# Kernel tuning notes

Measured on AMD Instinct MI355X. Metric: run time of the kernel, lower is better.

## Reference

```python
import jax, jax.numpy as jnp
import numpy as np

T, N, E, V, D, H, Dh = 64, 2048, 8192, 64000, 128, 12, 10  # head_size = 128 // 12 = 10


def setup_inputs() -> dict:
    key = jax.random.key(0)
    ks = jax.random.split(key, 16)
    s = 1.0 / np.sqrt(D)
    return {
        "node_ids": jax.random.randint(ks[0], (T, N), 0, V, dtype=jnp.int32),
        "src": jax.random.randint(ks[1], (T, E), 0, N, dtype=jnp.int32),
        "dst": jax.random.randint(ks[2], (T, E), 0, N, dtype=jnp.int32),
        "edge_weights": jax.random.uniform(ks[3], (T, E), dtype=jnp.float32),
        "emb": jax.random.normal(ks[4], (V, D), dtype=jnp.float32) * 0.02,
        "Wp": jax.random.normal(ks[5], (D, D), dtype=jnp.float32) * s,
        "bp": jnp.zeros((D,), jnp.float32),
        "Wq": jax.random.normal(ks[6], (D, H * Dh), dtype=jnp.float32) * s,
        "bq": jnp.zeros((H * Dh,), jnp.float32),
        "Wk": jax.random.normal(ks[7], (D, H * Dh), dtype=jnp.float32) * s,
        "bk": jnp.zeros((H * Dh,), jnp.float32),
        "Wv": jax.random.normal(ks[8], (D, H * Dh), dtype=jnp.float32) * s,
        "bv": jnp.zeros((H * Dh,), jnp.float32),
        "Wo": jax.random.normal(ks[9], (H * Dh, 2), dtype=jnp.float32) * (1.0 / np.sqrt(H * Dh)),
        "bo": jnp.zeros((2,), jnp.float32),
    }


def reference(node_ids, src, dst, edge_weights, emb, Wp, bp, Wq, bq, Wk, bk, Wv, bv, Wo, bo):
    def propagate(x, s, d, w):
        # edge-weighted gather-multiply-scatter-add, then linear projection
        msg = x[s] * w[:, None]                                   # [E, D]
        n_hat = x + jax.ops.segment_sum(msg, d, num_segments=N)   # [N, D]
        return n_hat @ Wp + bp

    def step(carry, inp):
        ids, s, d, w = inp
        x = emb[ids]                       # [N, D] embedding lookup
        x = propagate(x, s, d, w)
        x = propagate(x, s, d, w)
        x = propagate(x, s, d, w)          # three rounds, as in SpatialEncoding.forward
        return carry, x

    _, node_emb = jax.lax.scan(step, None, (node_ids, src, dst, edge_weights))  # [T, N, D]

    # per-node temporal sequence: [N, T, D]
    seq = jnp.transpose(node_emb, (1, 0, 2))

    q = (seq @ Wq + bq).reshape(N, T, H, Dh)
    k = (seq @ Wk + bk).reshape(N, T, H, Dh)
    v = (seq @ Wv + bv).reshape(N, T, H, Dh)

    scale = 1.0 / jnp.sqrt(jnp.float32(Dh))
    scores = jnp.einsum('nthd,nshd->nhts', q, k) * scale          # [N, H, T, T]
    attn = jax.nn.softmax(scores, axis=-1)
    out = jnp.einsum('nhts,nshd->nthd', attn, v).reshape(N, T, H * Dh)  # [N, T, 120]

    # agg = cat over nodes -> [N*T, 120]; transpose(1,0).mean(-1) == mean over N*T axis
    agg = out.reshape(N * T, H * Dh).mean(axis=0)                 # [120]
    return agg @ Wo + bo                                          # [2]
```

## Files before the change

kernel.cpp:

```cpp
#include <hip/hip_runtime.h>
#include <stdint.h>

#define TT 64
#define NN 2048
#define EE 8192
#define DD 128
#define CAP 32

typedef __attribute__((ext_vector_type(8))) short bvec8;
typedef __attribute__((ext_vector_type(4))) float fvec4;

__device__ __forceinline__ float bf2f(uint16_t u){
  union { uint32_t i; float f; } v; v.i = ((uint32_t)u) << 16; return v.f;
}
__device__ __forceinline__ float lo16(uint32_t u){
  union { uint32_t i; float f; } v; v.i = u << 16; return v.f;
}
__device__ __forceinline__ float hi16(uint32_t u){
  union { uint32_t i; float f; } v; v.i = u & 0xffff0000u; return v.f;
}
__device__ __forceinline__ uint16_t f2bf(float f){
  union { float f; uint32_t i; } v; v.f = f;
  uint32_t r = v.i + 0x7fffu + ((v.i >> 16) & 1u);
  return (uint16_t)(r >> 16);
}
__device__ __forceinline__ uint32_t cvtpk(float lo, float hi){
  uint32_t r;
  asm("v_cvt_pk_bf16_f32 %0, %1, %2" : "=v"(r) : "v"(lo), "v"(hi));
  return r;
}
__device__ __forceinline__ fvec4 mfma16(bvec8 a, bvec8 b, fvec4 c){
  return __builtin_amdgcn_mfma_f32_16x16x32_bf16(a, b, c, 0, 0, 0);
}
__device__ __forceinline__ bvec8 pack8z(float a, float b, float c, float d){
  union { uint32_t u[4]; bvec8 v; } r;
  r.u[0] = cvtpk(a, b);
  r.u[1] = cvtpk(c, d);
  r.u[2] = 0u;
  r.u[3] = 0u;
  return r.v;
}

__global__ void k_init(const int* __restrict__ dst, int* __restrict__ cnt,
                       int* __restrict__ esw,
                       const float* __restrict__ Wp, const float* __restrict__ Wq,
                       const float* __restrict__ Wk, const float* __restrict__ Wv,
                       const float* __restrict__ bq, const float* __restrict__ bk,
                       const float* __restrict__ bv,
                       uint16_t* __restrict__ WpHi, uint16_t* __restrict__ WpLo,
                       uint16_t* __restrict__ QHi, float* __restrict__ biasPad,
                       const int* __restrict__ ids, const float* __restrict__ emb,
                       uint16_t* __restrict__ x){
  int bid = blockIdx.x;
  if (bid < 2048){
    int tid = bid * 256 + threadIdx.x;
    int t = tid >> 13, e = tid & (EE - 1);
    int d = dst[tid];
    int row = t * NN + d;
    int pos = atomicAdd(&cnt[row], 1);
    if (pos < CAP) esw[(size_t)row * 2 * CAP + 2 * pos] = e;
  } else if (bid < 2048 + 47){
    int tid = (bid - 2048) * 256 + threadIdx.x;
    if (tid < 2048){
      int lane = tid & 63, kc = (tid >> 6) & 3, ct = tid >> 8;
      int g = lane >> 4, l15 = lane & 15;
      #pragma unroll
      for (int j = 0; j < 8; ++j){
        int k = kc * 32 + g * 8 + j;
        int col = ct * 16 + l15;
        float v = Wp[k * DD + col];
        uint16_t h = f2bf(v);
        WpHi[(size_t)tid * 8 + j] = h;
        WpLo[(size_t)tid * 8 + j] = f2bf(v - bf2f(h));
      }
    } else if (tid < 2048 + 9216){
      int idx = tid - 2048;
      int lane = idx & 63, kc = (idx >> 6) & 3, t2 = idx >> 8;
      int h = t2 % 12, m = t2 / 12;
      const float* W = (m == 0) ? Wq : (m == 1) ? Wk : Wv;
      int g = lane >> 4, l15 = lane & 15;
      #pragma unroll
      for (int j = 0; j < 8; ++j){
        int k = kc * 32 + g * 8 + j;
        float v = (l15 < 10) ? W[k * 120 + h * 10 + l15] : 0.f;
        QHi[(size_t)idx * 8 + j] = f2bf(v);
      }
    } else if (tid < 2048 + 9216 + 576){
      int idx = tid - (2048 + 9216);
      int m = idx / 192, rest = idx % 192;
      int h = rest / 16, d = rest % 16;
      const float* B = (m == 0) ? bq : (m == 1) ? bk : bv;
      biasPad[idx] = (d < 10) ? B[h * 10 + d] : 0.f;
    }
  } else {
    int tid = (bid - 2095) * 256 + threadIdx.x;
    int row = tid >> 4, c8 = tid & 15;
    int id = ids[row];
    const float* er = emb + (size_t)id * DD + c8 * 8;
    float4 a = *(const float4*)er;
    float4 b = *(const float4*)(er + 4);
    union { uint32_t u[4]; bvec8 v; } o;
    o.u[0] = cvtpk(a.x, a.y);
    o.u[1] = cvtpk(a.z, a.w);
    o.u[2] = cvtpk(b.x, b.y);
    o.u[3] = cvtpk(b.z, b.w);
    *(bvec8*)(x + (size_t)row * DD + c8 * 8) = o.v;
  }
}

__global__ void k_sortconv(int* __restrict__ cnt, int* __restrict__ esw,
                           const int* __restrict__ srcA, const float* __restrict__ ewA){
  int row = blockIdx.x * 256 + threadIdx.x;
  if (row >= TT * NN) return;
  int t = row >> 11;
  int c = cnt[row]; if (c > CAP) c = CAP;
  cnt[row] = c;
  int* p = esw + (size_t)row * 2 * CAP;
  for (int i = 0; i < c; ++i){
    int mi = i, mv = p[2 * i];
    for (int j = i + 1; j < c; ++j){ int vj = p[2 * j]; if (vj < mv){ mv = vj; mi = j; } }
    if (mi != i){ p[2 * mi] = p[2 * i]; p[2 * i] = mv; }
  }
  const int* srcT = srcA + (size_t)t * EE;
  const float* ewT = ewA + (size_t)t * EE;
  for (int i = 0; i < c; ++i){
    int e = p[2 * i];
    p[2 * i]     = srcT[e];
    p[2 * i + 1] = __float_as_int(ewT[e]);
  }
}

__global__ __launch_bounds__(256, 4) void k_prop(const uint16_t* __restrict__ xin,
    uint16_t* __restrict__ xout, const int* __restrict__ cnt, const int* __restrict__ esw,
    const uint16_t* __restrict__ WHi, const uint16_t* __restrict__ WLo,
    const float* __restrict__ bp, int topt){
  __shared__ uint16_t lds[64 * 136];
  __shared__ int4 eplds[256];
  int vb = blockIdx.x;
  int b = ((vb & 7) << 8) | (vb >> 3);
  int t = b >> 5, n0 = (b & 31) << 6;
  int tid = threadIdx.x, w = tid >> 6, lane = tid & 63, g = lane >> 4, l15 = lane & 15;
  const uint16_t* xt = xin + (size_t)t * NN * DD;
  int baseRow = t * NN + n0;
  eplds[tid] = ((const int4*)(esw + (size_t)(baseRow + (tid >> 2)) * 2 * CAP))[tid & 3];
  int myc = (lane < 16) ? cnt[baseRow + w * 16 + lane] : 0;
  __syncthreads();
  #pragma unroll 2
  for (int i = 0; i < 16; ++i){
    int r = w * 16 + i;
    int n = n0 + r;
    uint32_t u = *(const uint32_t*)(xt + (size_t)n * DD + (lane << 1));
    int c = __shfl(myc, i);
    const int4* epr = &eplds[r * 4];
    int4 q0 = epr[0], q1 = epr[1], q2 = epr[2], q3 = epr[3];
    int sj[8]   = {q0.x, q0.z, q1.x, q1.z, q2.x, q2.z, q3.x, q3.z};
    float wj[8] = {__int_as_float(q0.y), __int_as_float(q0.w),
                   __int_as_float(q1.y), __int_as_float(q1.w),
                   __int_as_float(q2.y), __int_as_float(q2.w),
                   __int_as_float(q3.y), __int_as_float(q3.w)};
    uint32_t xs[8];
    float wf[8];
    #pragma unroll
    for (int j = 0; j < 8; ++j){
      int s = (j < c) ? sj[j] : 0;
      wf[j] = (j < c) ? wj[j] : 0.f;
      xs[j] = *(const uint32_t*)(xt + (size_t)s * DD + (lane << 1));
    }
    float a0 = lo16(u);
    float a1 = hi16(u);
    #pragma unroll
    for (int j = 0; j < 8; ++j){
      a0 = fmaf(wf[j], lo16(xs[j]), a0);
      a1 = fmaf(wf[j], hi16(xs[j]), a1);
    }
    if (c > 8){
      int rowg = baseRow + r;
      for (int j = 8; j < c; ++j){
        int s = esw[(size_t)rowg * 2 * CAP + 2 * j];
        float wt = __int_as_float(esw[(size_t)rowg * 2 * CAP + 2 * j + 1]);
        uint32_t us = *(const uint32_t*)(xt + (size_t)s * DD + (lane << 1));
        a0 = fmaf(wt, lo16(us), a0);
        a1 = fmaf(wt, hi16(us), a1);
      }
    }
    *(uint32_t*)&lds[r * 136 + (lane << 1)] = cvtpk(a0, a1);
  }
  __syncthreads();
  bvec8 afr[4];
  int arow = w * 16 + l15;
  #pragma unroll
  for (int kc = 0; kc < 4; ++kc)
    afr[kc] = *(const bvec8*)&lds[arow * 136 + kc * 32 + g * 8];
  fvec4 acc[8];
  #pragma unroll
  for (int i = 0; i < 8; ++i) acc[i] = fvec4{0.f, 0.f, 0.f, 0.f};
  #pragma unroll
  for (int kc = 0; kc < 4; ++kc){
    #pragma unroll
    for (int ct = 0; ct < 8; ++ct){
      size_t base = ((size_t)(ct * 4 + kc) * 64 + lane) * 8;
      acc[ct] = mfma16(afr[kc], *(const bvec8*)&WHi[base], acc[ct]);
      acc[ct] = mfma16(afr[kc], *(const bvec8*)&WLo[base], acc[ct]);
    }
  }
  __syncthreads();
  #pragma unroll
  for (int ct = 0; ct < 8; ++ct){
    int col = ct * 16 + l15;
    float bias = bp[col];
    uint32_t c01 = cvtpk(acc[ct][0] + bias, acc[ct][1] + bias);
    uint32_t c23 = cvtpk(acc[ct][2] + bias, acc[ct][3] + bias);
    int r = w * 16 + g * 4;
    lds[(r + 0) * 136 + col] = (uint16_t)c01;
    lds[(r + 1) * 136 + col] = (uint16_t)(c01 >> 16);
    lds[(r + 2) * 136 + col] = (uint16_t)c23;
    lds[(r + 3) * 136 + col] = (uint16_t)(c23 >> 16);
  }
  __syncthreads();
  #pragma unroll
  for (int p = 0; p < 4; ++p){
    int chunk = p * 256 + tid, r = chunk >> 4, c8 = chunk & 15;
    bvec8 v = *(const bvec8*)&lds[r * 136 + c8 * 8];
    size_t dstoff;
    if (topt == 0) dstoff = ((size_t)t * NN + n0 + r) * DD + c8 * 8;
    else           dstoff = (((size_t)(n0 + r)) * TT + t) * DD + c8 * 8;
    *(bvec8*)(xout + dstoff) = v;
  }
}

__global__ __launch_bounds__(256, 3) void k_attn(const uint16_t* __restrict__ x3,
    const uint16_t* __restrict__ QHi, const float* __restrict__ biasPad,
    float* __restrict__ partials){
  __shared__ uint16_t seq[64 * 136];
  int n = blockIdx.x;
  int tid = threadIdx.x, w = tid >> 6, lane = tid & 63, g = lane >> 4, l15 = lane & 15;
  const uint16_t* xr = x3 + (size_t)n * TT * DD;
  #pragma unroll
  for (int p4 = 0; p4 < 4; ++p4){
    int chunk = p4 * 256 + tid, r = chunk >> 4, c8 = chunk & 15;
    *(bvec8*)&seq[r * 136 + c8 * 8] = *(const bvec8*)&xr[r * 128 + c8 * 8];
  }
  __syncthreads();

  const float CSC = 0.31622776601683794f * 1.4426950408889634f;

  for (int pass = 0; pass < 3; ++pass){
    int h = pass * 4 + w;
    bvec8 qf8[4], kf8[4], vf8[4];
    #pragma unroll
    for (int m = 0; m < 3; ++m){
      fvec4 acc[4];
      #pragma unroll
      for (int i = 0; i < 4; ++i) acc[i] = fvec4{0.f, 0.f, 0.f, 0.f};
      #pragma unroll
      for (int kc = 0; kc < 4; ++kc){
        bvec8 B = *(const bvec8*)&QHi[((size_t)((m * 12 + h) * 4 + kc) * 64 + lane) * 8];
        #pragma unroll
        for (int tb = 0; tb < 4; ++tb){
          bvec8 a = *(const bvec8*)&seq[(tb * 16 + l15) * 136 + kc * 32 + g * 8];
          if (m == 2) acc[tb] = mfma16(a, B, acc[tb]);
          else        acc[tb] = mfma16(B, a, acc[tb]);
        }
      }
      if (m == 0){
        float4 b4 = *(const float4*)&biasPad[(0 * 12 + h) * 16 + g * 4];
        #pragma unroll
        for (int tb = 0; tb < 4; ++tb)
          qf8[tb] = pack8z((acc[tb][0] + b4.x) * CSC, (acc[tb][1] + b4.y) * CSC,
                           (acc[tb][2] + b4.z) * CSC, (acc[tb][3] + b4.w) * CSC);
      } else if (m == 1){
        float4 b4 = *(const float4*)&biasPad[(1 * 12 + h) * 16 + g * 4];
        #pragma unroll
        for (int tb = 0; tb < 4; ++tb)
          kf8[tb] = pack8z(acc[tb][0] + b4.x, acc[tb][1] + b4.y,
                           acc[tb][2] + b4.z, acc[tb][3] + b4.w);
      } else {
        float bias = biasPad[(2 * 12 + h) * 16 + l15];
        #pragma unroll
        for (int tb = 0; tb < 4; ++tb)
          vf8[tb] = pack8z(acc[tb][0] + bias, acc[tb][1] + bias,
                           acc[tb][2] + bias, acc[tb][3] + bias);
      }
    }
    float csum = 0.f;
    #pragma unroll
    for (int tb = 0; tb < 4; ++tb){
      fvec4 p[4];
      #pragma unroll
      for (int sb = 0; sb < 4; ++sb)
        p[sb] = mfma16(kf8[sb], qf8[tb], fvec4{0.f, 0.f, 0.f, 0.f});
      float s = 0.f;
      #pragma unroll
      for (int sb = 0; sb < 4; ++sb)
        #pragma unroll
        for (int rg = 0; rg < 4; ++rg){
          float pv = exp2f(p[sb][rg]);
          p[sb][rg] = pv;
          s += pv;
        }
      s += __shfl_xor(s, 16);
      s += __shfl_xor(s, 32);
      float rinv = __builtin_amdgcn_rcpf(s);
      fvec4 o = fvec4{0.f, 0.f, 0.f, 0.f};
      #pragma unroll
      for (int sb = 0; sb < 4; ++sb){
        bvec8 pf = pack8z(p[sb][0] * rinv, p[sb][1] * rinv,
                          p[sb][2] * rinv, p[sb][3] * rinv);
        o = mfma16(pf, vf8[sb], o);
      }
      csum += o[0] + o[1] + o[2] + o[3];
    }
    csum += __shfl_xor(csum, 16);
    csum += __shfl_xor(csum, 32);
    if (g == 0 && l15 < 10)
      partials[(size_t)n * 120 + h * 10 + l15] = csum;
  }
}

__global__ void k_reduce(const float* __restrict__ partials, float* __restrict__ agg){
  __shared__ float red[256];
  int c = blockIdx.x, tid = threadIdx.x;
  float s = 0.f;
  for (int b = tid; b < NN; b += 256) s += partials[(size_t)b * 120 + c];
  red[tid] = s;
  __syncthreads();
  for (int st = 128; st > 0; st >>= 1){
    if (tid < st) red[tid] += red[tid + st];
    __syncthreads();
  }
  if (tid == 0) agg[c] = red[0] * (1.0f / (float)(NN * TT));
}

__global__ void k_final(const float* __restrict__ agg, const float* __restrict__ Wo,
                        const float* __restrict__ bo, float* __restrict__ out){
  __shared__ float r0[128], r1[128];
  int j = threadIdx.x;
  float a = (j < 120) ? agg[j] : 0.f;
  r0[j] = (j < 120) ? a * Wo[2 * j] : 0.f;
  r1[j] = (j < 120) ? a * Wo[2 * j + 1] : 0.f;
  __syncthreads();
  for (int st = 64; st > 0; st >>= 1){
    if (j < st){ r0[j] += r0[j + st]; r1[j] += r1[j + st]; }
    __syncthreads();
  }
  if (j == 0){ out[0] = r0[0] + bo[0]; out[1] = r1[0] + bo[1]; }
}

extern "C" void kernel_launch(void* const* d_in, const int* in_sizes, int n_in,
                              void* d_out, int out_size, void* d_ws, size_t ws_size,
                              hipStream_t stream){
  const int*   node_ids = (const int*)d_in[0];
  const int*   srcA     = (const int*)d_in[1];
  const int*   dstA     = (const int*)d_in[2];
  const float* ew       = (const float*)d_in[3];
  const float* emb      = (const float*)d_in[4];
  const float* Wp       = (const float*)d_in[5];
  const float* bp       = (const float*)d_in[6];
  const float* Wq       = (const float*)d_in[7];
  const float* bq       = (const float*)d_in[8];
  const float* Wk       = (const float*)d_in[9];
  const float* bk       = (const float*)d_in[10];
  const float* Wv       = (const float*)d_in[11];
  const float* bv       = (const float*)d_in[12];
  const float* Wo       = (const float*)d_in[13];
  const float* bo       = (const float*)d_in[14];

  char* p = (char*)d_ws;
  auto alloc = [&](size_t bytes) -> char* {
    char* r = p; p += (bytes + 255) & ~(size_t)255; return r;
  };
  uint16_t* xA    = (uint16_t*)alloc((size_t)TT * NN * DD * 2);
  uint16_t* xB    = (uint16_t*)alloc((size_t)TT * NN * DD * 2);
  int*      cnt   = (int*)alloc((size_t)TT * NN * 4);
  int*      esw   = (int*)alloc((size_t)TT * NN * 2 * CAP * 4);
  uint16_t* WpHi  = (uint16_t*)alloc(2048 * 8 * 2);
  uint16_t* WpLo  = (uint16_t*)alloc(2048 * 8 * 2);
  uint16_t* QHi   = (uint16_t*)alloc(9216 * 8 * 2);
  float*    biasP = (float*)alloc(576 * 4);
  float*    parts = (float*)alloc((size_t)NN * 120 * 4);
  float*    agg   = (float*)alloc(120 * 4);

  hipMemsetAsync(cnt, 0, (size_t)TT * NN * 4, stream);
  k_init<<<2048 + 47 + 8192, 256, 0, stream>>>(dstA, cnt, esw,
      Wp, Wq, Wk, Wv, bq, bk, bv, WpHi, WpLo, QHi, biasP,
      node_ids, emb, xA);
  k_sortconv<<<TT * NN / 256, 256, 0, stream>>>(cnt, esw, srcA, ew);
  k_prop<<<2048, 256, 0, stream>>>(xA, xB, cnt, esw, WpHi, WpLo, bp, 0);
  k_prop<<<2048, 256, 0, stream>>>(xB, xA, cnt, esw, WpHi, WpLo, bp, 0);
  k_prop<<<2048, 256, 0, stream>>>(xA, xB, cnt, esw, WpHi, WpLo, bp, 1);
  k_attn<<<NN, 256, 0, stream>>>(xB, QHi, biasP, parts);
  k_reduce<<<120, 256, 0, stream>>>(parts, agg);
  k_final<<<1, 128, 0, stream>>>(agg, Wo, bo, (float*)d_out);
}
```

Before: 261.4 us.

## Shrink k_prop tiles to 16 rows per block and split MFMA columns across waves

k_prop now handles 16 nodes per block instead of 64, launching 8192 blocks. Each wave gathers 4 rows, and the projection GEMM is split so each wave computes 32 output columns of the shared 16-row tile rather than a full 16x128 tile. LDS per block and accumulator registers shrink, and the launch bound rises to 6 blocks per SIMD to increase occupancy and latency hiding for the gather. In exchange, each weight fragment is reloaded across four times as many blocks. Separately, k_attn's launch bound occupancy hint is raised from 3 to 4.

```diff
diff --git a/kernel.cpp b/kernel.cpp
--- a/kernel.cpp
+++ b/kernel.cpp
@@ -130,27 +130,28 @@
   }
 }
 
-__global__ __launch_bounds__(256, 4) void k_prop(const uint16_t* __restrict__ xin,
+__global__ __launch_bounds__(256, 6) void k_prop(const uint16_t* __restrict__ xin,
     uint16_t* __restrict__ xout, const int* __restrict__ cnt, const int* __restrict__ esw,
     const uint16_t* __restrict__ WHi, const uint16_t* __restrict__ WLo,
     const float* __restrict__ bp, int topt){
-  __shared__ uint16_t lds[64 * 136];
-  __shared__ int4 eplds[256];
+  __shared__ uint16_t lds[16 * 136];
+  __shared__ int4 eplds[64];
   int vb = blockIdx.x;
-  int b = ((vb & 7) << 8) | (vb >> 3);
-  int t = b >> 5, n0 = (b & 31) << 6;
+  int b = ((vb & 7) << 10) | (vb >> 3);
+  int t = b >> 7, n0 = (b & 127) << 4;
   int tid = threadIdx.x, w = tid >> 6, lane = tid & 63, g = lane >> 4, l15 = lane & 15;
   const uint16_t* xt = xin + (size_t)t * NN * DD;
   int baseRow = t * NN + n0;
-  eplds[tid] = ((const int4*)(esw + (size_t)(baseRow + (tid >> 2)) * 2 * CAP))[tid & 3];
-  int myc = (lane < 16) ? cnt[baseRow + w * 16 + lane] : 0;
+  if (tid < 64)
+    eplds[tid] = ((const int4*)(esw + (size_t)(baseRow + (tid >> 2)) * 2 * CAP))[tid & 3];
+  int myc = (lane < 16) ? cnt[baseRow + lane] : 0;
   __syncthreads();
   #pragma unroll 2
-  for (int i = 0; i < 16; ++i){
-    int r = w * 16 + i;
+  for (int i = 0; i < 4; ++i){
+    int r = w * 4 + i;
     int n = n0 + r;
     uint32_t u = *(const uint32_t*)(xt + (size_t)n * DD + (lane << 1));
-    int c = __shfl(myc, i);
+    int c = __shfl(myc, r);
     const int4* epr = &eplds[r * 4];
     int4 q0 = epr[0], q1 = epr[1], q2 = epr[2], q3 = epr[3];
     int sj[8]   = {q0.x, q0.z, q1.x, q1.z, q2.x, q2.z, q3.x, q3.z};
@@ -187,39 +188,38 @@
   }
   __syncthreads();
   bvec8 afr[4];
-  int arow = w * 16 + l15;
   #pragma unroll
   for (int kc = 0; kc < 4; ++kc)
-    afr[kc] = *(const bvec8*)&lds[arow * 136 + kc * 32 + g * 8];
-  fvec4 acc[8];
-  #pragma unroll
-  for (int i = 0; i < 8; ++i) acc[i] = fvec4{0.f, 0.f, 0.f, 0.f};
+    afr[kc] = *(const bvec8*)&lds[l15 * 136 + kc * 32 + g * 8];
+  fvec4 acc[2];
+  acc[0] = fvec4{0.f, 0.f, 0.f, 0.f};
+  acc[1] = fvec4{0.f, 0.f, 0.f, 0.f};
   #pragma unroll
   for (int kc = 0; kc < 4; ++kc){
     #pragma unroll
-    for (int ct = 0; ct < 8; ++ct){
+    for (int c2 = 0; c2 < 2; ++c2){
+      int ct = w * 2 + c2;
       size_t base = ((size_t)(ct * 4 + kc) * 64 + lane) * 8;
-      acc[ct] = mfma16(afr[kc], *(const bvec8*)&WHi[base], acc[ct]);
-      acc[ct] = mfma16(afr[kc], *(const bvec8*)&WLo[base], acc[ct]);
+      acc[c2] = mfma16(afr[kc], *(const bvec8*)&WHi[base], acc[c2]);
+      acc[c2] = mfma16(afr[kc], *(const bvec8*)&WLo[base], acc[c2]);
     }
   }
   __syncthreads();
   #pragma unroll
-  for (int ct = 0; ct < 8; ++ct){
-    int col = ct * 16 + l15;
+  for (int c2 = 0; c2 < 2; ++c2){
+    int col = (w * 2 + c2) * 16 + l15;
     float bias = bp[col];
-    uint32_t c01 = cvtpk(acc[ct][0] + bias, acc[ct][1] + bias);
-    uint32_t c23 = cvtpk(acc[ct][2] + bias, acc[ct][3] + bias);
-    int r = w * 16 + g * 4;
+    uint32_t c01 = cvtpk(acc[c2][0] + bias, acc[c2][1] + bias);
+    uint32_t c23 = cvtpk(acc[c2][2] + bias, acc[c2][3] + bias);
+    int r = g * 4;
     lds[(r + 0) * 136 + col] = (uint16_t)c01;
     lds[(r + 1) * 136 + col] = (uint16_t)(c01 >> 16);
     lds[(r + 2) * 136 + col] = (uint16_t)c23;
     lds[(r + 3) * 136 + col] = (uint16_t)(c23 >> 16);
   }
   __syncthreads();
-  #pragma unroll
-  for (int p = 0; p < 4; ++p){
-    int chunk = p * 256 + tid, r = chunk >> 4, c8 = chunk & 15;
+  {
+    int r = tid >> 4, c8 = tid & 15;
     bvec8 v = *(const bvec8*)&lds[r * 136 + c8 * 8];
     size_t dstoff;
     if (topt == 0) dstoff = ((size_t)t * NN + n0 + r) * DD + c8 * 8;
@@ -228,7 +228,7 @@
   }
 }
 
-__global__ __launch_bounds__(256, 3) void k_attn(const uint16_t* __restrict__ x3,
+__global__ __launch_bounds__(256, 4) void k_attn(const uint16_t* __restrict__ x3,
     const uint16_t* __restrict__ QHi, const float* __restrict__ biasPad,
     float* __restrict__ partials){
   __shared__ uint16_t seq[64 * 136];
@@ -385,9 +385,9 @@
       Wp, Wq, Wk, Wv, bq, bk, bv, WpHi, WpLo, QHi, biasP,
       node_ids, emb, xA);
   k_sortconv<<<TT * NN / 256, 256, 0, stream>>>(cnt, esw, srcA, ew);
-  k_prop<<<2048, 256, 0, stream>>>(xA, xB, cnt, esw, WpHi, WpLo, bp, 0);
-  k_prop<<<2048, 256, 0, stream>>>(xB, xA, cnt, esw, WpHi, WpLo, bp, 0);
-  k_prop<<<2048, 256, 0, stream>>>(xA, xB, cnt, esw, WpHi, WpLo, bp, 1);
+  k_prop<<<8192, 256, 0, stream>>>(xA, xB, cnt, esw, WpHi, WpLo, bp, 0);
+  k_prop<<<8192, 256, 0, stream>>>(xB, xA, cnt, esw, WpHi, WpLo, bp, 0);
+  k_prop<<<8192, 256, 0, stream>>>(xA, xB, cnt, esw, WpHi, WpLo, bp, 1);
   k_attn<<<NN, 256, 0, stream>>>(xB, QHi, biasP, parts);
   k_reduce<<<120, 256, 0, stream>>>(parts, agg);
   k_final<<<1, 128, 0, stream>>>(agg, Wo, bo, (float*)d_out);
```

After: 262.7 us. No clear change (+0.5%).
